# Kernel tuning notes

Measured on AMD Instinct MI355X. Metric: run time of the kernel, lower is better.

Reference implementation:

```python
import jax, jax.numpy as jnp
import numpy as np

B, N, H, S, C = 32, 64, 128, 100, 16
SIGMA = 0.5  # perturbations.perturbed default noise scale


def setup_inputs() -> dict:
    key = jax.random.key(0)
    ks = jax.random.split(key, 8)
    x = jax.random.normal(ks[0], (B, N, H), jnp.float32)
    a = (jax.random.uniform(ks[1], (B, N, N)) < 0.1).astype(jnp.float32)
    adj = jnp.maximum(a, jnp.swapaxes(a, -1, -2))  # symmetric binary adjacency
    counts = jax.random.randint(ks[2], (B,), N // 2, N + 1)
    mask = jnp.arange(N)[None, :] < counts[:, None]
    sc = 1.0 / np.sqrt(H).astype(np.float32)
    W1 = jax.random.normal(ks[3], (H, H), jnp.float32) * sc
    b1 = jnp.zeros((H,), jnp.float32)
    W2 = jax.random.normal(ks[4], (H, H), jnp.float32) * sc
    b2 = jnp.zeros((H,), jnp.float32)
    cW1 = jax.random.normal(ks[5], (H, H), jnp.float32) * sc
    cb1 = jnp.zeros((H,), jnp.float32)
    cW2 = jax.random.normal(ks[6], (H, C), jnp.float32) * sc
    cb2 = jnp.zeros((C,), jnp.float32)
    noise = jax.random.normal(ks[7], (S * B, N, H), jnp.float32)
    return dict(x=x, adj=adj, mask=mask, W1=W1, b1=b1, W2=W2, b2=b2,
                cW1=cW1, cb1=cb1, cW2=cW2, cb2=cb2, noise=noise, num_samples=S)


def _gcn(x, adj, mask, W, b):
    # DenseGCNConv: set diag to 1, symmetric-normalize, propagate, mask.
    h = x @ W
    n = adj.shape[-1]
    eye = jnp.eye(n, dtype=bool)
    a = jnp.where(eye, 1.0, adj)
    d = jnp.clip(a.sum(-1), 1.0, None) ** -0.5
    a = d[..., :, None] * a * d[..., None, :]
    out = a @ h + b
    return out * mask[..., None].astype(out.dtype)


def _perturbed_clustering(x_all, adj_all, mask_all, cW1, cb1, cW2, cb2):
    BS, n, h = x_all.shape
    # concept MLP + argmax
    logits = jax.nn.relu(x_all @ cW1 + cb1) @ cW2 + cb2
    concepts = jnp.argmax(logits, axis=-1)  # [BS, n]
    same = concepts[:, :, None] == concepts[:, None, :]
    adj_c = jnp.where(same, adj_all, 0.0)
    # connected components via min-label propagation (scipy-order relabel)
    edge = (adj_c > 0) & mask_all[:, :, None] & mask_all[:, None, :]
    labels0 = jnp.where(mask_all, jnp.arange(n, dtype=jnp.int32), n)

    def body(_, labels):
        neigh = jnp.min(jnp.where(edge, labels[:, None, :], n), axis=-1)
        return jnp.minimum(labels, neigh)

    roots = jax.lax.fori_loop(0, n, body, labels0)  # min node idx of component
    present = jnp.zeros((BS, n + 1), jnp.int32).at[
        jnp.arange(BS)[:, None], roots].max(mask_all.astype(jnp.int32))
    rank = jnp.cumsum(present[:, :n], axis=-1)  # 1-based compact id per root
    assignments = jnp.where(
        mask_all,
        jnp.take_along_axis(rank, jnp.minimum(roots, n - 1), axis=-1), 0)
    # scatter-reduce pooling; segment ids flatten (batch, cluster); slot 0 = masked
    seg = (jnp.arange(BS, dtype=jnp.int32)[:, None] * (n + 1) + assignments).reshape(-1)
    x_new = jax.ops.segment_sum(x_all.reshape(BS * n, h), seg,
                                num_segments=BS * (n + 1)).reshape(BS, n + 1, h)[:, 1:]
    row = jax.ops.segment_max(adj_all.reshape(BS * n, n), seg,
                              num_segments=BS * (n + 1)).reshape(BS, n + 1, n)[:, 1:]
    row = jnp.maximum(row, 0.0)  # torch_scatter max includes zero-init
    colsrc = jnp.swapaxes(row, 1, 2).reshape(BS * n, n)
    adj_new = jax.ops.segment_max(colsrc, seg,
                                  num_segments=BS * (n + 1)).reshape(BS, n + 1, n)[:, 1:]
    adj_new = jnp.maximum(jnp.swapaxes(adj_new, 1, 2), 0.0)
    num_clusters = jnp.max(assignments, axis=-1)
    mask_new = jnp.arange(n)[None, :] < num_clusters[:, None]
    return x_new, adj_new, mask_new, assignments


def reference(x, adj, mask, W1, b1, W2, b2, cW1, cb1, cW2, cb2, noise, num_samples):
    # embedding GCN stack
    xe = jax.nn.relu(_gcn(x, adj, mask, W1, b1))
    x_emb = jax.nn.relu(_gcn(xe, adj, mask, W2, b2))
    Bb, n, h = x_emb.shape
    # perturbed replication (sample-major layout, matching final reshape(S, -1, ...))
    adj_all = jnp.tile(adj, (num_samples, 1, 1))
    mask_all = jnp.tile(mask, (num_samples, 1))
    x_all = jnp.tile(x_emb, (num_samples, 1, 1)) + SIGMA * noise
    x_new, adj_new, mask_new, assignments = _perturbed_clustering(
        x_all, adj_all, mask_all, cW1, cb1, cW2, cb2)
    # perturbed expectation for x_new; explicit mean/max in forward for adj/mask
    x_new = x_new.reshape(num_samples, Bb, n, h).mean(axis=0)
    adj_new = adj_new.reshape(num_samples, Bb, n, n).mean(axis=0)
    mask_new = jnp.max(mask_new.reshape(num_samples, Bb, n), axis=0)
    return x_new, adj_new, assignments, x_emb, mask_new
```

## Files before the change

kernel.cpp:

```cpp
#include <hip/hip_runtime.h>
#include <cstdint>

#define B_ 32
#define N_ 64
#define H_ 128
#define S_ 100
#define C_ 16
#define SIGMA_ 0.5f

#define OFF_XNEW 0
#define OFF_ADJN 262144
#define OFF_ASGN 393216
#define OFF_XEMB 598016
#define OFF_MSKN 860160

__device__ __forceinline__ int read_mask_elem(const void* mp, int idx) {
    const unsigned int* u = (const unsigned int*)mp;
    const unsigned int w0 = u[0], w1 = u[1];
    if (w0 == 1u) {
        if (w1 == 1u) return ((const int*)mp)[idx] != 0;
        return ((const int*)mp)[2 * idx] != 0;
    }
    if (w0 == 0x3f800000u) return ((const float*)mp)[idx] != 0.0f;
    if (w0 == 0u) return ((const double*)mp)[idx] != 0.0;
    return ((const unsigned char*)mp)[idx] != 0;
}

__global__ __launch_bounds__(256) void gcn_kernel(
    const float* __restrict__ x, const float* __restrict__ adj,
    const void* __restrict__ maskp,
    const float* __restrict__ W1, const float* __restrict__ b1,
    const float* __restrict__ W2, const float* __restrict__ b2,
    float* __restrict__ out,
    unsigned long long* __restrict__ abits_ws,
    unsigned long long* __restrict__ mbits_ws)
{
    const int b = blockIdx.x;
    const int t = threadIdx.x;
    __shared__ float Xs[N_][130];
    __shared__ float Hs[N_][130];
    __shared__ float An[N_][65];
    __shared__ float dsh[N_];
    __shared__ unsigned long long mb_sh;

    if (t < 64) {
        const int mv = read_mask_elem(maskp, b * N_ + t);
        const unsigned long long bal = __ballot(mv != 0);
        if (t == 0) { mb_sh = bal; mbits_ws[b] = bal; }
    }
    for (int row = (t >> 6); row < N_; row += 4) {
        const int j = t & 63;
        const float v = adj[((size_t)b * N_ + row) * N_ + j];
        const unsigned long long bal = __ballot(v > 0.0f);
        if (j == 0) abits_ws[b * N_ + row] = bal;
        An[row][j] = (row == j) ? 1.0f : v;
    }
    __syncthreads();
    if (t < 64) {
        float s = 0.0f;
        for (int j = 0; j < N_; ++j) s += An[t][j];
        if (s < 1.0f) s = 1.0f;
        dsh[t] = 1.0f / sqrtf(s);
    }
    __syncthreads();
    for (int e = t; e < N_ * N_; e += 256) {
        const int i = e >> 6, j = e & 63;
        An[i][j] *= dsh[i] * dsh[j];
    }
    for (int e = t; e < N_ * H_; e += 256)
        Xs[e >> 7][e & 127] = x[(size_t)b * N_ * H_ + e];
    __syncthreads();

    const int ng = t & 15, kg = t >> 4;
    const unsigned long long mb = mb_sh;

    {
        float acc[4][8] = {};
        for (int d = 0; d < H_; ++d) {
            float xv[4];
#pragma unroll
            for (int r = 0; r < 4; ++r) xv[r] = Xs[4 * ng + r][d];
            const float4 wa = *(const float4*)(W1 + d * H_ + 8 * kg);
            const float4 wb = *(const float4*)(W1 + d * H_ + 8 * kg + 4);
            const float wf[8] = {wa.x, wa.y, wa.z, wa.w, wb.x, wb.y, wb.z, wb.w};
#pragma unroll
            for (int j = 0; j < 8; ++j)
#pragma unroll
                for (int r = 0; r < 4; ++r) acc[r][j] += xv[r] * wf[j];
        }
#pragma unroll
        for (int r = 0; r < 4; ++r)
#pragma unroll
            for (int j = 0; j < 8; ++j) Hs[4 * ng + r][8 * kg + j] = acc[r][j];
    }
    __syncthreads();
    {
        float acc[4][8] = {};
        for (int j2 = 0; j2 < N_; ++j2) {
            float av[4];
#pragma unroll
            for (int r = 0; r < 4; ++r) av[r] = An[4 * ng + r][j2];
            float hv[8];
#pragma unroll
            for (int j = 0; j < 8; ++j) hv[j] = Hs[j2][8 * kg + j];
#pragma unroll
            for (int j = 0; j < 8; ++j)
#pragma unroll
                for (int r = 0; r < 4; ++r) acc[r][j] += av[r] * hv[j];
        }
        const float4 ba = *(const float4*)(b1 + 8 * kg);
        const float4 bb = *(const float4*)(b1 + 8 * kg + 4);
        const float bf[8] = {ba.x, ba.y, ba.z, ba.w, bb.x, bb.y, bb.z, bb.w};
#pragma unroll
        for (int r = 0; r < 4; ++r) {
            const int i = 4 * ng + r;
            const float m = ((mb >> i) & 1ull) ? 1.0f : 0.0f;
#pragma unroll
            for (int j = 0; j < 8; ++j)
                Xs[i][8 * kg + j] = fmaxf(acc[r][j] + bf[j], 0.0f) * m;
        }
    }
    __syncthreads();
    {
        float acc[4][8] = {};
        for (int d = 0; d < H_; ++d) {
            float xv[4];
#pragma unroll
            for (int r = 0; r < 4; ++r) xv[r] = Xs[4 * ng + r][d];
            const float4 wa = *(const float4*)(W2 + d * H_ + 8 * kg);
            const float4 wb = *(const float4*)(W2 + d * H_ + 8 * kg + 4);
            const float wf[8] = {wa.x, wa.y, wa.z, wa.w, wb.x, wb.y, wb.z, wb.w};
#pragma unroll
            for (int j = 0; j < 8; ++j)
#pragma unroll
                for (int r = 0; r < 4; ++r) acc[r][j] += xv[r] * wf[j];
        }
        __syncthreads();
#pragma unroll
        for (int r = 0; r < 4; ++r)
#pragma unroll
            for (int j = 0; j < 8; ++j) Hs[4 * ng + r][8 * kg + j] = acc[r][j];
    }
    __syncthreads();
    {
        float acc[4][8] = {};
        for (int j2 = 0; j2 < N_; ++j2) {
            float av[4];
#pragma unroll
            for (int r = 0; r < 4; ++r) av[r] = An[4 * ng + r][j2];
            float hv[8];
#pragma unroll
            for (int j = 0; j < 8; ++j) hv[j] = Hs[j2][8 * kg + j];
#pragma unroll
            for (int j = 0; j < 8; ++j)
#pragma unroll
                for (int r = 0; r < 4; ++r) acc[r][j] += av[r] * hv[j];
        }
        const float4 ba = *(const float4*)(b2 + 8 * kg);
        const float4 bb = *(const float4*)(b2 + 8 * kg + 4);
        const float bf[8] = {ba.x, ba.y, ba.z, ba.w, bb.x, bb.y, bb.z, bb.w};
#pragma unroll
        for (int r = 0; r < 4; ++r) {
            const int i = 4 * ng + r;
            const float m = ((mb >> i) & 1ull) ? 1.0f : 0.0f;
#pragma unroll
            for (int j = 0; j < 8; ++j)
                out[OFF_XEMB + (size_t)b * N_ * H_ + i * H_ + 8 * kg + j] =
                    fmaxf(acc[r][j] + bf[j], 0.0f) * m;
        }
    }
}

__global__ __launch_bounds__(256) void sample_kernel(
    const float* __restrict__ noise,
    const float* __restrict__ cW1, const float* __restrict__ cb1,
    const float* __restrict__ cW2, const float* __restrict__ cb2,
    const unsigned long long* __restrict__ abits_ws,
    const unsigned long long* __restrict__ mbits_ws,
    float* __restrict__ out, int* __restrict__ gNcl)
{
    const int sb = blockIdx.x;
    const int b  = sb & (B_ - 1);
    const int t  = threadIdx.x;
    __shared__ float xa[N_ * H_];
    __shared__ float hid[N_ * H_];
    __shared__ int   concepts[N_];
    __shared__ int   a_lds[N_];
    __shared__ unsigned long long reachL[N_];
    __shared__ unsigned long long cmS[N_];
    __shared__ unsigned long long roS[N_];
    __shared__ unsigned long long abS[N_];
    __shared__ unsigned int presLo, presHi;

    const unsigned long long mb = mbits_ws[b];
    if (t < 64) abS[t] = abits_ws[b * N_ + t];
    if (t == 0) { presLo = 0u; presHi = 0u; }

    {
        const float4* e4 = (const float4*)(out + OFF_XEMB + (size_t)b * N_ * H_);
        const float4* n4 = (const float4*)(noise + (size_t)sb * N_ * H_);
        float4* x4 = (float4*)xa;
        for (int idx = t; idx < N_ * 32; idx += 256) {
            const int i = idx >> 5, cc = idx & 31;
            const float4 ev = e4[idx], nv = n4[idx];
            float4 v;
            v.x = ev.x + SIGMA_ * nv.x;  v.y = ev.y + SIGMA_ * nv.y;
            v.z = ev.z + SIGMA_ * nv.z;  v.w = ev.w + SIGMA_ * nv.w;
            x4[i * 32 + (cc ^ ((i >> 2) & 7))] = v;
        }
    }
    __syncthreads();

    {
        const int ng = t & 15, kg = t >> 4;
        float acc[4][8] = {};
        const float4* x4 = (const float4*)xa;
        for (int cc = 0; cc < 32; ++cc) {
            float xv[4][4];
#pragma unroll
            for (int r = 0; r < 4; ++r) {
                const float4 tmp = x4[(4 * ng + r) * 32 + (cc ^ (ng & 7))];
                xv[r][0] = tmp.x; xv[r][1] = tmp.y; xv[r][2] = tmp.z; xv[r][3] = tmp.w;
            }
#pragma unroll
            for (int dd = 0; dd < 4; ++dd) {
                const int d = cc * 4 + dd;
                const float4 wa = *(const float4*)(cW1 + d * H_ + 8 * kg);
                const float4 wb = *(const float4*)(cW1 + d * H_ + 8 * kg + 4);
                const float wf[8] = {wa.x, wa.y, wa.z, wa.w, wb.x, wb.y, wb.z, wb.w};
#pragma unroll
                for (int j = 0; j < 8; ++j)
#pragma unroll
                    for (int r = 0; r < 4; ++r) acc[r][j] += xv[r][dd] * wf[j];
            }
        }
        const float4 ba = *(const float4*)(cb1 + 8 * kg);
        const float4 bb = *(const float4*)(cb1 + 8 * kg + 4);
        const float bf[8] = {ba.x, ba.y, ba.z, ba.w, bb.x, bb.y, bb.z, bb.w};
#pragma unroll
        for (int r = 0; r < 4; ++r) {
            const int i = 4 * ng + r;
            const int swz = ng & 7;
            float4 o0, o1;
            o0.x = fmaxf(acc[r][0] + bf[0], 0.f); o0.y = fmaxf(acc[r][1] + bf[1], 0.f);
            o0.z = fmaxf(acc[r][2] + bf[2], 0.f); o0.w = fmaxf(acc[r][3] + bf[3], 0.f);
            o1.x = fmaxf(acc[r][4] + bf[4], 0.f); o1.y = fmaxf(acc[r][5] + bf[5], 0.f);
            o1.z = fmaxf(acc[r][6] + bf[6], 0.f); o1.w = fmaxf(acc[r][7] + bf[7], 0.f);
            *(float4*)&hid[i * H_ + (((2 * kg)     ^ swz) << 2)] = o0;
            *(float4*)&hid[i * H_ + (((2 * kg + 1) ^ swz) << 2)] = o1;
        }
    }
    __syncthreads();

    {
        const int node = t >> 2, q = t & 3;
        const int h = (node >> 2) & 7;
        float acc[C_] = {};
        for (int kk = 0; kk < 32; ++kk) {
            const int k = 4 * kk + q;
            const float hv = hid[node * H_ + ((kk ^ h) << 2) + q];
            const float4 w0 = *(const float4*)(cW2 + k * C_);
            const float4 w1 = *(const float4*)(cW2 + k * C_ + 4);
            const float4 w2 = *(const float4*)(cW2 + k * C_ + 8);
            const float4 w3 = *(const float4*)(cW2 + k * C_ + 12);
            acc[0]  += hv * w0.x; acc[1]  += hv * w0.y; acc[2]  += hv * w0.z; acc[3]  += hv * w0.w;
            acc[4]  += hv * w1.x; acc[5]  += hv * w1.y; acc[6]  += hv * w1.z; acc[7]  += hv * w1.w;
            acc[8]  += hv * w2.x; acc[9]  += hv * w2.y; acc[10] += hv * w2.z; acc[11] += hv * w2.w;
            acc[12] += hv * w3.x; acc[13] += hv * w3.y; acc[14] += hv * w3.z; acc[15] += hv * w3.w;
        }
#pragma unroll
        for (int c = 0; c < C_; ++c) {
            acc[c] += __shfl_xor(acc[c], 1);
            acc[c] += __shfl_xor(acc[c], 2);
        }
        if (q == 0) {
            float best = acc[0] + cb2[0]; int bi = 0;
#pragma unroll
            for (int c = 1; c < C_; ++c) {
                const float v = acc[c] + cb2[c];
                if (v > best) { best = v; bi = c; }
            }
            concepts[node] = bi;
        }
    }
    __syncthreads();

    unsigned long long reach = 0ull;
    int masked_i = 0;
    if (t < 64) {
        masked_i = (int)((mb >> t) & 1ull);
        if (masked_i) {
            const int ci = concepts[t];
            unsigned long long mm = abS[t] & mb;
            unsigned long long em = 0ull;
            while (mm) {
                const int j = __builtin_ctzll(mm);
                if (concepts[j] == ci) em |= (1ull << j);
                mm &= mm - 1;
            }
            reach = em | (1ull << t);
        }
        reachL[t] = reach;
    }
    __syncthreads();
#pragma unroll 1
    for (int it = 0; it < 6; ++it) {
        unsigned long long r = reach;
        if (masked_i) {
            unsigned long long mm = reach;
            while (mm) {
                const int j = __builtin_ctzll(mm);
                r |= reachL[j];
                mm &= mm - 1;
            }
        }
        __syncthreads();
        if (t < 64) reachL[t] = r;
        reach = r;
        __syncthreads();
    }
    int root = 0;
    if (masked_i) {
        root = __builtin_ctzll(reach);
        if (root < 32) atomicOr(&presLo, 1u << root);
        else           atomicOr(&presHi, 1u << (root - 32));
    }
    __syncthreads();
    const unsigned long long present =
        ((unsigned long long)presHi << 32) | (unsigned long long)presLo;
    const int ncl = __popcll(present);
    if (t < 64) {
        int a_i = 0;
        if (masked_i) {
            a_i = __popcll(present & ((1ull << root) - 1ull)) + 1;
            if (root == t) {
                cmS[a_i - 1] = reach;
                unsigned long long ro = 0ull, mm = reach;
                while (mm) { const int j = __builtin_ctzll(mm); ro |= abS[j]; mm &= mm - 1; }
                roS[a_i - 1] = ro;
            }
        }
        a_lds[t] = a_i;
        out[OFF_ASGN + (size_t)sb * N_ + t] = (float)a_i;
    }
    __syncthreads();

    {
        int* adjCnt = (int*)out + OFF_ADJN;
        for (int idx = t; idx < N_ * N_; idx += 256) {
            const int c1 = idx >> 6, c2 = idx & 63;
            if (c1 < ncl && c2 < ncl && (roS[c1] & cmS[c2]))
                atomicAdd(&adjCnt[b * N_ * N_ + idx], 1);
        }
    }
    for (int e = t; e < N_ * H_; e += 256) hid[e] = 0.0f;
    __syncthreads();
    for (int e = t; e < N_ * H_; e += 256) {
        const int i = e >> 7, d = e & 127;
        const int a = a_lds[i];
        if (a) {
            const float v = xa[i * H_ + ((((d >> 2) ^ ((i >> 2) & 7)) << 2) | (d & 3))];
            atomicAdd(&hid[(a - 1) * H_ + d], v);
        }
    }
    __syncthreads();
    for (int e = t; e < ncl * H_; e += 256)
        atomicAdd(&out[OFF_XNEW + (size_t)b * N_ * H_ + e], hid[e]);
    if (t == 0) atomicMax(&gNcl[b], ncl);
}

__global__ __launch_bounds__(256) void finalize_kernel(
    float* __restrict__ out, const int* __restrict__ gNcl)
{
    const int idx = blockIdx.x * 256 + threadIdx.x;
    if (idx < OFF_ADJN) {
        out[idx] = out[idx] / 100.0f;
    } else if (idx < OFF_ASGN) {
        const int c = ((const int*)out)[idx];
        out[idx] = (float)c / 100.0f;
    } else {
        const int m = idx - OFF_ASGN;
        if (m < B_ * N_) {
            const int bb = m >> 6, k = m & 63;
            out[OFF_MSKN + m] = (k < gNcl[bb]) ? 1.0f : 0.0f;
        }
    }
}

extern "C" void kernel_launch(void* const* d_in, const int* in_sizes, int n_in,
                              void* d_out, int out_size, void* d_ws, size_t ws_size,
                              hipStream_t stream) {
    (void)in_sizes; (void)n_in; (void)out_size; (void)ws_size;
    const float* x    = (const float*)d_in[0];
    const float* adj  = (const float*)d_in[1];
    const void*  mskp = d_in[2];
    const float* W1   = (const float*)d_in[3];
    const float* b1   = (const float*)d_in[4];
    const float* W2   = (const float*)d_in[5];
    const float* b2   = (const float*)d_in[6];
    const float* cW1  = (const float*)d_in[7];
    const float* cb1  = (const float*)d_in[8];
    const float* cW2  = (const float*)d_in[9];
    const float* cb2  = (const float*)d_in[10];
    const float* noise = (const float*)d_in[11];
    float* out = (float*)d_out;

    int* gNcl = (int*)d_ws;
    unsigned long long* abits_ws = (unsigned long long*)((char*)d_ws + 256);
    unsigned long long* mbits_ws = (unsigned long long*)((char*)d_ws + 256 + 16384);

    hipMemsetAsync(d_out, 0, (size_t)OFF_ASGN * sizeof(float), stream);
    hipMemsetAsync(d_ws, 0, 256, stream);

    gcn_kernel<<<B_, 256, 0, stream>>>(x, adj, mskp, W1, b1, W2, b2,
                                       out, abits_ws, mbits_ws);
    sample_kernel<<<S_ * B_, 256, 0, stream>>>(noise, cW1, cb1, cW2, cb2,
                                               abits_ws, mbits_ws, out, gNcl);
    finalize_kernel<<<(OFF_ASGN + B_ * N_ + 255) / 256, 256, 0, stream>>>(out, gNcl);
}
```

Baseline: 526.2 us.

## Fuse concept MLP layers in registers, early-exit reachability, gather cluster sums

```diff
diff --git a/kernel.cpp b/kernel.cpp
--- a/kernel.cpp
+++ b/kernel.cpp
@@ -171,7 +171,45 @@
     }
 }
 
-__global__ __launch_bounds__(256) void sample_kernel(
+__device__ __forceinline__ float rscat16(float* v, int kg) {
+#pragma unroll
+    for (int i = 0; i < 8; ++i) {
+        const float send = (kg & 8) ? v[i] : v[i + 8];
+        const float recv = __shfl_xor(send, 8);
+        v[i] = ((kg & 8) ? v[i + 8] : v[i]) + recv;
+    }
+#pragma unroll
+    for (int i = 0; i < 4; ++i) {
+        const float send = (kg & 4) ? v[i] : v[i + 4];
+        const float recv = __shfl_xor(send, 4);
+        v[i] = ((kg & 4) ? v[i + 4] : v[i]) + recv;
+    }
+#pragma unroll
+    for (int i = 0; i < 2; ++i) {
+        const float send = (kg & 2) ? v[i] : v[i + 2];
+        const float recv = __shfl_xor(send, 2);
+        v[i] = ((kg & 2) ? v[i + 2] : v[i]) + recv;
+    }
+    {
+        const float send = (kg & 1) ? v[0] : v[1];
+        const float recv = __shfl_xor(send, 1);
+        v[0] = ((kg & 1) ? v[1] : v[0]) + recv;
+    }
+    return v[0];
+}
+
+__device__ __forceinline__ void argmax16(float bv, int kg, int* dst) {
+    int bi = kg;
+#pragma unroll
+    for (int m = 1; m <= 8; m <<= 1) {
+        const float ov = __shfl_xor(bv, m);
+        const int   oi = __shfl_xor(bi, m);
+        if (ov > bv || (ov == bv && oi < bi)) { bv = ov; bi = oi; }
+    }
+    if (kg == 0) *dst = bi;
+}
+
+__global__ __launch_bounds__(256, 4) void sample_kernel(
     const float* __restrict__ noise,
     const float* __restrict__ cW1, const float* __restrict__ cb1,
     const float* __restrict__ cW2, const float* __restrict__ cb2,
@@ -183,9 +221,7 @@
     const int b  = sb & (B_ - 1);
     const int t  = threadIdx.x;
     __shared__ float xa[N_ * H_];
-    __shared__ float hid[N_ * H_];
     __shared__ int   concepts[N_];
-    __shared__ int   a_lds[N_];
     __shared__ unsigned long long reachL[N_];
     __shared__ unsigned long long cmS[N_];
     __shared__ unsigned long long roS[N_];
@@ -206,20 +242,21 @@
             float4 v;
             v.x = ev.x + SIGMA_ * nv.x;  v.y = ev.y + SIGMA_ * nv.y;
             v.z = ev.z + SIGMA_ * nv.z;  v.w = ev.w + SIGMA_ * nv.w;
-            x4[i * 32 + (cc ^ ((i >> 2) & 7))] = v;
-        }
-    }
-    __syncthreads();
-
-    {
-        const int ng = t & 15, kg = t >> 4;
-        float acc[4][8] = {};
+            x4[i * 32 + (cc ^ (i & 7))] = v;
+        }
+    }
+    __syncthreads();
+
+    const int ng = t >> 4, kg = t & 15;
+    float acc[4][8] = {};
+    {
         const float4* x4 = (const float4*)xa;
+        const int swzb = 4 * (ng & 1);
         for (int cc = 0; cc < 32; ++cc) {
             float xv[4][4];
 #pragma unroll
             for (int r = 0; r < 4; ++r) {
-                const float4 tmp = x4[(4 * ng + r) * 32 + (cc ^ (ng & 7))];
+                const float4 tmp = x4[(4 * ng + r) * 32 + (cc ^ (swzb + r))];
                 xv[r][0] = tmp.x; xv[r][1] = tmp.y; xv[r][2] = tmp.z; xv[r][3] = tmp.w;
             }
 #pragma unroll
@@ -234,53 +271,37 @@
                     for (int r = 0; r < 4; ++r) acc[r][j] += xv[r][dd] * wf[j];
             }
         }
+    }
+    {
         const float4 ba = *(const float4*)(cb1 + 8 * kg);
         const float4 bb = *(const float4*)(cb1 + 8 * kg + 4);
         const float bf[8] = {ba.x, ba.y, ba.z, ba.w, bb.x, bb.y, bb.z, bb.w};
-#pragma unroll
-        for (int r = 0; r < 4; ++r) {
-            const int i = 4 * ng + r;
-            const int swz = ng & 7;
-            float4 o0, o1;
-            o0.x = fmaxf(acc[r][0] + bf[0], 0.f); o0.y = fmaxf(acc[r][1] + bf[1], 0.f);
-            o0.z = fmaxf(acc[r][2] + bf[2], 0.f); o0.w = fmaxf(acc[r][3] + bf[3], 0.f);
-            o1.x = fmaxf(acc[r][4] + bf[4], 0.f); o1.y = fmaxf(acc[r][5] + bf[5], 0.f);
-            o1.z = fmaxf(acc[r][6] + bf[6], 0.f); o1.w = fmaxf(acc[r][7] + bf[7], 0.f);
-            *(float4*)&hid[i * H_ + (((2 * kg)     ^ swz) << 2)] = o0;
-            *(float4*)&hid[i * H_ + (((2 * kg + 1) ^ swz) << 2)] = o1;
-        }
-    }
-    __syncthreads();
-
-    {
-        const int node = t >> 2, q = t & 3;
-        const int h = (node >> 2) & 7;
-        float acc[C_] = {};
-        for (int kk = 0; kk < 32; ++kk) {
-            const int k = 4 * kk + q;
-            const float hv = hid[node * H_ + ((kk ^ h) << 2) + q];
-            const float4 w0 = *(const float4*)(cW2 + k * C_);
-            const float4 w1 = *(const float4*)(cW2 + k * C_ + 4);
-            const float4 w2 = *(const float4*)(cW2 + k * C_ + 8);
-            const float4 w3 = *(const float4*)(cW2 + k * C_ + 12);
-            acc[0]  += hv * w0.x; acc[1]  += hv * w0.y; acc[2]  += hv * w0.z; acc[3]  += hv * w0.w;
-            acc[4]  += hv * w1.x; acc[5]  += hv * w1.y; acc[6]  += hv * w1.z; acc[7]  += hv * w1.w;
-            acc[8]  += hv * w2.x; acc[9]  += hv * w2.y; acc[10] += hv * w2.z; acc[11] += hv * w2.w;
-            acc[12] += hv * w3.x; acc[13] += hv * w3.y; acc[14] += hv * w3.z; acc[15] += hv * w3.w;
-        }
-#pragma unroll
-        for (int c = 0; c < C_; ++c) {
-            acc[c] += __shfl_xor(acc[c], 1);
-            acc[c] += __shfl_xor(acc[c], 2);
-        }
-        if (q == 0) {
-            float best = acc[0] + cb2[0]; int bi = 0;
-#pragma unroll
-            for (int c = 1; c < C_; ++c) {
-                const float v = acc[c] + cb2[c];
-                if (v > best) { best = v; bi = c; }
-            }
-            concepts[node] = bi;
+        const float cb2v = cb2[kg];
+#pragma unroll 1
+        for (int pp = 0; pp < 2; ++pp) {
+            float h0[8], h1[8];
+#pragma unroll
+            for (int j = 0; j < 8; ++j) {
+                h0[j] = fmaxf(acc[2 * pp][j] + bf[j], 0.0f);
+                h1[j] = fmaxf(acc[2 * pp + 1][j] + bf[j], 0.0f);
+            }
+            float pl0[16] = {}, pl1[16] = {};
+#pragma unroll
+            for (int j = 0; j < 8; ++j) {
+                const float4* w2r = (const float4*)(cW2 + (8 * kg + j) * C_);
+                const float4 w0 = w2r[0], w1 = w2r[1], w2v = w2r[2], w3 = w2r[3];
+                const float wf2[16] = {w0.x, w0.y, w0.z, w0.w, w1.x, w1.y, w1.z, w1.w,
+                                       w2v.x, w2v.y, w2v.z, w2v.w, w3.x, w3.y, w3.z, w3.w};
+#pragma unroll
+                for (int c = 0; c < C_; ++c) {
+                    pl0[c] += h0[j] * wf2[c];
+                    pl1[c] += h1[j] * wf2[c];
+                }
+            }
+            const float l0 = rscat16(pl0, kg) + cb2v;
+            const float l1 = rscat16(pl1, kg) + cb2v;
+            argmax16(l0, kg, &concepts[4 * ng + 2 * pp]);
+            argmax16(l1, kg, &concepts[4 * ng + 2 * pp + 1]);
         }
     }
     __syncthreads();
@@ -303,21 +324,21 @@
         reachL[t] = reach;
     }
     __syncthreads();
-#pragma unroll 1
-    for (int it = 0; it < 6; ++it) {
+    for (;;) {
         unsigned long long r = reach;
         if (masked_i) {
-            unsigned long long mm = reach;
+            unsigned long long mm = reach & ~(1ull << t);
             while (mm) {
                 const int j = __builtin_ctzll(mm);
                 r |= reachL[j];
                 mm &= mm - 1;
             }
         }
+        const int changed = (r != reach);
         __syncthreads();
         if (t < 64) reachL[t] = r;
         reach = r;
-        __syncthreads();
+        if (!__syncthreads_or(changed)) break;
     }
     int root = 0;
     if (masked_i) {
@@ -340,32 +361,29 @@
                 roS[a_i - 1] = ro;
             }
         }
-        a_lds[t] = a_i;
         out[OFF_ASGN + (size_t)sb * N_ + t] = (float)a_i;
     }
     __syncthreads();
 
+    for (int e = t; e < ncl * H_; e += 256) {
+        const int c = e >> 7, d = e & 127;
+        unsigned long long mm = cmS[c];
+        float s = 0.0f;
+        while (mm) {
+            const int j = __builtin_ctzll(mm);
+            s += xa[j * H_ + ((((d >> 2) ^ (j & 7)) << 2) | (d & 3))];
+            mm &= mm - 1;
+        }
+        atomicAdd(&out[OFF_XNEW + (size_t)b * N_ * H_ + e], s);
+    }
     {
         int* adjCnt = (int*)out + OFF_ADJN;
-        for (int idx = t; idx < N_ * N_; idx += 256) {
+        for (int idx = t; idx < ncl * N_; idx += 256) {
             const int c1 = idx >> 6, c2 = idx & 63;
-            if (c1 < ncl && c2 < ncl && (roS[c1] & cmS[c2]))
+            if (c2 < ncl && (roS[c1] & cmS[c2]))
                 atomicAdd(&adjCnt[b * N_ * N_ + idx], 1);
         }
     }
-    for (int e = t; e < N_ * H_; e += 256) hid[e] = 0.0f;
-    __syncthreads();
-    for (int e = t; e < N_ * H_; e += 256) {
-        const int i = e >> 7, d = e & 127;
-        const int a = a_lds[i];
-        if (a) {
-            const float v = xa[i * H_ + ((((d >> 2) ^ ((i >> 2) & 7)) << 2) | (d & 3))];
-            atomicAdd(&hid[(a - 1) * H_ + d], v);
-        }
-    }
-    __syncthreads();
-    for (int e = t; e < ncl * H_; e += 256)
-        atomicAdd(&out[OFF_XNEW + (size_t)b * N_ * H_ + e], hid[e]);
     if (t == 0) atomicMax(&gNcl[b], ncl);
 }
 
```

Measured after the change: 637.1 us. +21.1%, slower.
